# Kernel tuning notes

Measured on AMD Instinct MI355X. Metric: run time of the kernel, lower is better.

## Reference

```python
import jax, jax.numpy as jnp
import numpy as np

BETA = 0.25
EPS = 1e-12

def normalise(x):
    # L2 normalise over last axis
    return x / jnp.sqrt(jnp.sum(x * x, axis=-1, keepdims=True) + EPS)

def setup_inputs() -> dict:
    key = jax.random.key(0)
    k = jax.random.split(key, 6)
    N, d, c, P = 8192, 768, 256, 16384
    return {
        "z": jax.random.normal(k[0], (N, d), dtype=jnp.float32),
        "W_in": jax.random.normal(k[1], (d, c), dtype=jnp.float32) * 0.02,
        "b_in": jnp.zeros((c,), dtype=jnp.float32),
        "W_out": jax.random.normal(k[2], (c, d), dtype=jnp.float32) * 0.02,
        "b_out": jnp.zeros((d,), dtype=jnp.float32),
        "codebook": jax.random.normal(k[3], (P, c), dtype=jnp.float32),
    }

def reference(z, W_in, b_in, W_out, b_out, codebook):
    sg = jax.lax.stop_gradient
    # input projection + L2 normalise
    zq = normalise(z @ W_in + b_in)                 # [N, c]
    cb = normalise(codebook)                        # [P, c]
    # squared euclidean distances: ||z||^2 - 2 z.c + ||c||^2
    dist = (jnp.sum(zq * zq, axis=-1, keepdims=True)
            - 2.0 * jnp.einsum('nc,pc->np', zq, cb)
            + jnp.sum(cb * cb, axis=-1)[None, :])   # [N, P]
    idxes = jnp.argmin(dist, axis=-1)               # [N]
    codes = normalise(codebook[idxes])              # gather + normalise, [N, c]
    loss = BETA * (zq - sg(codes)) ** 2 + (sg(zq) - codes) ** 2
    # straight-through estimator
    codes = zq + sg(codes - zq)
    out = codes @ W_out + b_out                     # [N, d]
    return out, loss, idxes
```

## Files before the change

kernel.cpp:

```cpp
#include <hip/hip_runtime.h>
#include <hip/hip_fp16.h>
#include <math.h>

#define NN 8192
#define DD 768
#define CC 256
#define PP 16384
#define NG 256
#define MARGIN 5.0e-3f
#define BETA_C 1.25f
#define EPS_C 1e-12f

typedef __attribute__((ext_vector_type(8))) _Float16 f16x8;
typedef __attribute__((ext_vector_type(8))) short bf16x8;
typedef __attribute__((ext_vector_type(4))) float f32x4;
typedef __attribute__((ext_vector_type(16))) float f32x16;

static __device__ __forceinline__ ushort f2h(float x) {
    _Float16 h = (_Float16)x;
    return __builtin_bit_cast(unsigned short, h);
}
static __device__ __forceinline__ ushort f2bf(float x) {
    unsigned u = __float_as_uint(x);
    return (ushort)((u + 0x7fffu + ((u >> 16) & 1u)) >> 16);
}
static __device__ __forceinline__ float bf2f(ushort h) {
    return __uint_as_float(((unsigned)h) << 16);
}

static __device__ __forceinline__ void gload_lds16(const void* g, void* l) {
    __builtin_amdgcn_global_load_lds(
        (const __attribute__((address_space(1))) unsigned int*)g,
        (__attribute__((address_space(3))) unsigned int*)l, 16, 0, 0);
}

__global__ __launch_bounds__(256) void k_gemm_in(const float* __restrict__ z,
    const float* __restrict__ W, const float* __restrict__ b,
    float* __restrict__ zq)
{
    __shared__ float zt[64][36];
    __shared__ float wt[32][68];
    const int t = threadIdx.x;
    const int ti = t >> 4, tj = t & 15;
    const int n0 = blockIdx.x * 64;
    const int c0 = blockIdx.y * 64;

    f32x4 acc[4];
#pragma unroll
    for (int r = 0; r < 4; ++r) acc[r] = (f32x4){0.f, 0.f, 0.f, 0.f};

    for (int k0 = 0; k0 < DD; k0 += 32) {
        __syncthreads();
#pragma unroll
        for (int l = 0; l < 2; ++l) {
            int idx = l * 256 + t;
            int row = idx >> 3, c4 = idx & 7;
            *reinterpret_cast<float4*>(&zt[row][c4 * 4]) =
                *reinterpret_cast<const float4*>(&z[(size_t)(n0 + row) * DD + k0 + c4 * 4]);
            int krow = idx >> 4, w4 = idx & 15;
            *reinterpret_cast<float4*>(&wt[krow][w4 * 4]) =
                *reinterpret_cast<const float4*>(&W[(size_t)(k0 + krow) * CC + c0 + w4 * 4]);
        }
        __syncthreads();
#pragma unroll
        for (int kk = 0; kk < 32; kk += 4) {
            float4 a4[4], b4[4];
#pragma unroll
            for (int r = 0; r < 4; ++r)
                a4[r] = *reinterpret_cast<const float4*>(&zt[ti * 4 + r][kk]);
#pragma unroll
            for (int q = 0; q < 4; ++q)
                b4[q] = *reinterpret_cast<const float4*>(&wt[kk + q][tj * 4]);
#pragma unroll
            for (int q = 0; q < 4; ++q)
#pragma unroll
                for (int r = 0; r < 4; ++r) {
                    float av = ((const float*)&a4[r])[q];
                    acc[r].x += av * b4[q].x;
                    acc[r].y += av * b4[q].y;
                    acc[r].z += av * b4[q].z;
                    acc[r].w += av * b4[q].w;
                }
        }
    }
#pragma unroll
    for (int r = 0; r < 4; ++r) {
        int col = c0 + tj * 4;
        float4 o;
        o.x = acc[r].x + b[col];
        o.y = acc[r].y + b[col + 1];
        o.z = acc[r].z + b[col + 2];
        o.w = acc[r].w + b[col + 3];
        *reinterpret_cast<float4*>(&zq[(size_t)(n0 + ti * 4 + r) * CC + col]) = o;
    }
}

__global__ __launch_bounds__(256) void k_norm2(const float* __restrict__ src,
    float* __restrict__ dstf32, ushort* __restrict__ dsth,
    float* __restrict__ sq, float* __restrict__ rinvout, int rows)
{
    const int wave = threadIdx.x >> 6;
    const int lane = threadIdx.x & 63;
    const int row = blockIdx.x * 4 + wave;
    if (row >= rows) return;
    float4 v = *reinterpret_cast<const float4*>(&src[(size_t)row * CC + lane * 4]);
    float s = v.x * v.x + v.y * v.y + v.z * v.z + v.w * v.w;
#pragma unroll
    for (int off = 32; off; off >>= 1) s += __shfl_xor(s, off, 64);
    float r = 1.0f / sqrtf(s + EPS_C);
    v.x *= r; v.y *= r; v.z *= r; v.w *= r;
    if (dstf32)
        *reinterpret_cast<float4*>(&dstf32[(size_t)row * CC + lane * 4]) = v;
    ushort4 hv;
    hv.x = f2h(v.x); hv.y = f2h(v.y); hv.z = f2h(v.z); hv.w = f2h(v.w);
    *reinterpret_cast<ushort4*>(&dsth[(size_t)row * CC + lane * 4]) = hv;
    if (sq) {
        float s2 = v.x * v.x + v.y * v.y + v.z * v.z + v.w * v.w;
#pragma unroll
        for (int off = 32; off; off >>= 1) s2 += __shfl_xor(s2, off, 64);
        if (lane == 0) {
            sq[row] = s2;
            if (rinvout) rinvout[row] = r;
        }
    }
}

__global__ __launch_bounds__(256) void k_split_w(const float* __restrict__ W,
    ushort* __restrict__ wthi, ushort* __restrict__ wtlo)
{
    __shared__ float tile[64][68];
    const int t = threadIdx.x;
    const int d0 = blockIdx.x * 64;
    const int k0 = blockIdx.y * 64;
#pragma unroll
    for (int i = 0; i < 16; ++i) {
        int row = i * 4 + (t >> 6);
        int col = t & 63;
        tile[row][col] = W[(size_t)(k0 + row) * DD + d0 + col];
    }
    __syncthreads();
#pragma unroll
    for (int i = 0; i < 16; ++i) {
        int drow = i * 4 + (t >> 6);
        int kc = t & 63;
        float v = tile[kc][drow];
        ushort hi = f2bf(v);
        float rres = v - bf2f(hi);
        ushort lo = f2bf(rres);
        wthi[(size_t)(d0 + drow) * CC + k0 + kc] = hi;
        wtlo[(size_t)(d0 + drow) * CC + k0 + kc] = lo;
    }
}

__global__ __launch_bounds__(256) void k_dist(
    const ushort* __restrict__ cbh, const ushort* __restrict__ zqh,
    const float* __restrict__ cz2,
    float* __restrict__ gmin, unsigned long long* __restrict__ maskA)
{
    __shared__ ushort lA[256 * 64];
    __shared__ ushort lB[128 * 64];
    const int t = threadIdx.x;
    const int lane = t & 63;
    const int w = t >> 6;
    const int wr = w >> 1;
    const int wc = w & 1;
    const int p0 = blockIdx.x * 256;
    const int n0 = blockIdx.y * 128;
    const int kh = lane >> 5;
    const int r31 = lane & 31;

    f32x16 acc[4][2];
#pragma unroll
    for (int mi = 0; mi < 4; ++mi) {
        const int pbm = p0 + wr * 128 + mi * 32;
#pragma unroll
        for (int q = 0; q < 4; ++q) {
            float4 cz = *reinterpret_cast<const float4*>(&cz2[pbm + q * 8 + kh * 4]);
#pragma unroll
            for (int j = 0; j < 4; ++j) {
                float v = -0.5f * ((const float*)&cz.x)[j];
                acc[mi][0][q * 4 + j] = v;
                acc[mi][1][q * 4 + j] = v;
            }
        }
    }

    const int srow = lane >> 3;
    const int schunk = (lane & 7) ^ srow;
    const char* srcA = (const char*)cbh + (size_t)(p0 + w * 64 + srow) * (CC * 2) + schunk * 16;
    const char* srcB = (const char*)zqh + (size_t)(n0 + w * 32 + srow) * (CC * 2) + schunk * 16;
    char* dstA = (char*)lA + (w * 64) * 128;
    char* dstB = (char*)lB + (w * 32) * 128;

    const char* lAc = (const char*)lA;
    const char* lBc = (const char*)lB;
    const int sx = (r31 & 7) << 4;

    for (int k0 = 0; k0 < CC; k0 += 64) {
        __syncthreads();
#pragma unroll
        for (int i = 0; i < 8; ++i)
            gload_lds16(srcA + (size_t)i * 8 * (CC * 2) + k0 * 2, dstA + i * 1024);
#pragma unroll
        for (int i = 0; i < 4; ++i)
            gload_lds16(srcB + (size_t)i * 8 * (CC * 2) + k0 * 2, dstB + i * 1024);
        __syncthreads();
#pragma unroll
        for (int ks = 0; ks < 4; ++ks) {
            const int ko = ((ks * 32 + kh * 16) ^ sx);
            f16x8 af[4], bfv[2];
#pragma unroll
            for (int mi = 0; mi < 4; ++mi)
                af[mi] = *reinterpret_cast<const f16x8*>(
                    lAc + (wr * 128 + mi * 32 + r31) * 128 + ko);
#pragma unroll
            for (int ni = 0; ni < 2; ++ni)
                bfv[ni] = *reinterpret_cast<const f16x8*>(
                    lBc + (wc * 64 + ni * 32 + r31) * 128 + ko);
#pragma unroll
            for (int mi = 0; mi < 4; ++mi)
#pragma unroll
                for (int ni = 0; ni < 2; ++ni)
                    acc[mi][ni] = __builtin_amdgcn_mfma_f32_32x32x16_f16(
                        af[mi], bfv[ni], acc[mi][ni], 0, 0, 0);
        }
    }

#pragma unroll
    for (int ni = 0; ni < 2; ++ni) {
#pragma unroll
        for (int g = 0; g < 2; ++g) {
            float M = -1e30f;
#pragma unroll
            for (int m2 = 0; m2 < 2; ++m2)
#pragma unroll
                for (int r = 0; r < 16; ++r) M = fmaxf(M, acc[g * 2 + m2][ni][r]);
            M = fmaxf(M, __shfl_xor(M, 32, 64));
            const float thr = M - 0.5f * MARGIN;
            unsigned long long msk = 0ull;
#pragma unroll
            for (int m2 = 0; m2 < 2; ++m2)
#pragma unroll
                for (int q = 0; q < 4; ++q) {
                    unsigned nib = 0u;
#pragma unroll
                    for (int j = 0; j < 4; ++j)
                        nib |= (acc[g * 2 + m2][ni][q * 4 + j] >= thr) ? (1u << j) : 0u;
                    msk |= (unsigned long long)nib << (m2 * 32 + q * 8 + kh * 4);
                }
            msk |= __shfl_xor(msk, 32, 64);
            if (kh == 0) {
                int n = n0 + wc * 64 + ni * 32 + r31;
                int grp = (p0 >> 6) + wr * 2 + g;
                gmin[(size_t)n * NG + grp] = -2.0f * M;
                maskA[(size_t)n * NG + grp] = msk;
            }
        }
    }
}

__global__ __launch_bounds__(256) void k_pick(
    const float* __restrict__ gmin, const unsigned long long* __restrict__ maskA,
    const float* __restrict__ zqn, const float* __restrict__ cb_raw,
    const float* __restrict__ rinv, const float* __restrict__ cz2,
    float* __restrict__ idxf, int* __restrict__ idxi)
{
    __shared__ int lst[4][256];
    __shared__ int cnt[4];
    const int t = threadIdx.x;
    const int w = t >> 6;
    const int lane = t & 63;
    const int row = blockIdx.x * 4 + w;

    float4 zr = *reinterpret_cast<const float4*>(&zqn[(size_t)row * CC + lane * 4]);
    float4 gv = *reinterpret_cast<const float4*>(&gmin[(size_t)row * NG + lane * 4]);

    float pm = fminf(fminf(gv.x, gv.y), fminf(gv.z, gv.w));
#pragma unroll
    for (int off = 1; off < 64; off <<= 1) pm = fminf(pm, __shfl_xor(pm, off, 64));
    const float thresh = pm + MARGIN;

    if (lane == 0) cnt[w] = 0;
    __syncthreads();
    {
        const float g4[4] = {gv.x, gv.y, gv.z, gv.w};
#pragma unroll
        for (int j = 0; j < 4; ++j)
            if (g4[j] <= thresh) {
                int pos = atomicAdd(&cnt[w], 1);
                lst[w][pos] = lane * 4 + j;
            }
    }
    __syncthreads();

    const int nc = cnt[w];
    unsigned long long best = ~0ull;
    for (int ci = 0; ci < nc; ++ci) {
        int g = lst[w][ci];
        unsigned long long msk = maskA[(size_t)row * NG + g];
        while (msk) {
            int bit = __ffsll((long long)msk) - 1;
            msk &= msk - 1;
            int p = g * 64 + bit;
            float rv = rinv[p];
            float4 c4 = *reinterpret_cast<const float4*>(&cb_raw[(size_t)p * CC + lane * 4]);
            float part = (c4.x * rv) * zr.x + (c4.y * rv) * zr.y
                       + (c4.z * rv) * zr.z + (c4.w * rv) * zr.w;
#pragma unroll
            for (int off = 1; off < 64; off <<= 1) part += __shfl_xor(part, off, 64);
            float d4 = fmaf(-2.0f, part, 4.0f + cz2[p]);
            unsigned long long pk = ((unsigned long long)__float_as_uint(d4) << 32) | (unsigned)p;
            best = best < pk ? best : pk;
        }
    }
    if (lane == 0) {
        int p = (int)(best & 0xffffffffu);
        idxf[row] = (float)p;
        idxi[row] = p;
    }
}

__global__ __launch_bounds__(256) void k_codes(const float* __restrict__ zqn,
    const float* __restrict__ cb_raw, const float* __restrict__ rinv,
    const int* __restrict__ idxv, ushort* __restrict__ chi,
    ushort* __restrict__ clo, float* __restrict__ loss)
{
    int idx = blockIdx.x * 256 + threadIdx.x;
    int n = idx >> 6;
    int c4 = idx & 63;
    int p = idxv[n];
    float rv = rinv[p];
    float4 cv = *reinterpret_cast<const float4*>(&cb_raw[(size_t)p * CC + c4 * 4]);
    cv.x *= rv; cv.y *= rv; cv.z *= rv; cv.w *= rv;
    ushort4 hv, lv16;
    {
        hv.x = f2bf(cv.x); lv16.x = f2bf(cv.x - bf2f(hv.x));
        hv.y = f2bf(cv.y); lv16.y = f2bf(cv.y - bf2f(hv.y));
        hv.z = f2bf(cv.z); lv16.z = f2bf(cv.z - bf2f(hv.z));
        hv.w = f2bf(cv.w); lv16.w = f2bf(cv.w - bf2f(hv.w));
    }
    *reinterpret_cast<ushort4*>(&chi[(size_t)n * CC + c4 * 4]) = hv;
    *reinterpret_cast<ushort4*>(&clo[(size_t)n * CC + c4 * 4]) = lv16;
    float4 zv = *reinterpret_cast<const float4*>(&zqn[(size_t)n * CC + c4 * 4]);
    float4 lsv;
    float dx = zv.x - cv.x, dy = zv.y - cv.y, dz = zv.z - cv.z, dw = zv.w - cv.w;
    lsv.x = BETA_C * dx * dx; lsv.y = BETA_C * dy * dy;
    lsv.z = BETA_C * dz * dz; lsv.w = BETA_C * dw * dw;
    *reinterpret_cast<float4*>(&loss[(size_t)n * CC + c4 * 4]) = lsv;
}

__global__ __launch_bounds__(256) void k_gemm_out_mfma(
    const ushort* __restrict__ chi, const ushort* __restrict__ clo,
    const ushort* __restrict__ wthi, const ushort* __restrict__ wtlo,
    const float* __restrict__ bout, float* __restrict__ out)
{
    __shared__ ushort sAh[128 * 64];
    __shared__ ushort sAl[128 * 64];
    __shared__ ushort sBh[128 * 64];
    __shared__ ushort sBl[128 * 64];
    const int t = threadIdx.x;
    const int lane = t & 63;
    const int w = t >> 6;
    const int wr = w >> 1;
    const int wc = w & 1;
    const int nb = blockIdx.x * 128;
    const int db = blockIdx.y * 128;
    const int kh = lane >> 5;
    const int r31 = lane & 31;

    f32x16 acc[2][2];
#pragma unroll
    for (int mi = 0; mi < 2; ++mi)
#pragma unroll
        for (int ni = 0; ni < 2; ++ni)
#pragma unroll
            for (int r = 0; r < 16; ++r) acc[mi][ni][r] = 0.f;

    const int srow = lane >> 3;
    const int schunk = (lane & 7) ^ srow;
    const size_t rowA = (size_t)(nb + w * 32 + srow) * CC;
    const size_t rowB = (size_t)(db + w * 32 + srow) * CC;
    const char* sAhsrc = (const char*)chi + rowA * 2 + schunk * 16;
    const char* sAlsrc = (const char*)clo + rowA * 2 + schunk * 16;
    const char* sBhsrc = (const char*)wthi + rowB * 2 + schunk * 16;
    const char* sBlsrc = (const char*)wtlo + rowB * 2 + schunk * 16;
    char* dA = (char*)sAh + (w * 32) * 128;
    char* dAl = (char*)sAl + (w * 32) * 128;
    char* dB = (char*)sBh + (w * 32) * 128;
    char* dBl = (char*)sBl + (w * 32) * 128;

    const int sx = (r31 & 7) << 4;

    for (int k0 = 0; k0 < CC; k0 += 64) {
        __syncthreads();
#pragma unroll
        for (int i = 0; i < 4; ++i) {
            gload_lds16(sAhsrc + (size_t)i * 8 * (CC * 2) + k0 * 2, dA + i * 1024);
            gload_lds16(sAlsrc + (size_t)i * 8 * (CC * 2) + k0 * 2, dAl + i * 1024);
            gload_lds16(sBhsrc + (size_t)i * 8 * (CC * 2) + k0 * 2, dB + i * 1024);
            gload_lds16(sBlsrc + (size_t)i * 8 * (CC * 2) + k0 * 2, dBl + i * 1024);
        }
        __syncthreads();
#pragma unroll
        for (int ks = 0; ks < 4; ++ks) {
            const int ko = ((ks * 32 + kh * 16) ^ sx);
            bf16x8 ah[2], al[2], bh[2], bl[2];
#pragma unroll
            for (int mi = 0; mi < 2; ++mi) {
                ah[mi] = *reinterpret_cast<const bf16x8*>(
                    (const char*)sAh + (wr * 64 + mi * 32 + r31) * 128 + ko);
                al[mi] = *reinterpret_cast<const bf16x8*>(
                    (const char*)sAl + (wr * 64 + mi * 32 + r31) * 128 + ko);
            }
#pragma unroll
            for (int ni = 0; ni < 2; ++ni) {
                bh[ni] = *reinterpret_cast<const bf16x8*>(
                    (const char*)sBh + (wc * 64 + ni * 32 + r31) * 128 + ko);
                bl[ni] = *reinterpret_cast<const bf16x8*>(
                    (const char*)sBl + (wc * 64 + ni * 32 + r31) * 128 + ko);
            }
#pragma unroll
            for (int mi = 0; mi < 2; ++mi)
#pragma unroll
                for (int ni = 0; ni < 2; ++ni) {
                    acc[mi][ni] = __builtin_amdgcn_mfma_f32_32x32x16_bf16(
                        ah[mi], bh[ni], acc[mi][ni], 0, 0, 0);
                    acc[mi][ni] = __builtin_amdgcn_mfma_f32_32x32x16_bf16(
                        ah[mi], bl[ni], acc[mi][ni], 0, 0, 0);
                    acc[mi][ni] = __builtin_amdgcn_mfma_f32_32x32x16_bf16(
                        al[mi], bh[ni], acc[mi][ni], 0, 0, 0);
                }
        }
    }

#pragma unroll
    for (int ni = 0; ni < 2; ++ni) {
        const int d = db + wc * 64 + ni * 32 + r31;
        const float bv = bout[d];
#pragma unroll
        for (int mi = 0; mi < 2; ++mi) {
            const int nbase = nb + wr * 64 + mi * 32 + 4 * kh;
#pragma unroll
            for (int q = 0; q < 4; ++q)
#pragma unroll
                for (int j = 0; j < 4; ++j) {
                    int n = nbase + j + 8 * q;
                    out[(size_t)n * DD + d] = acc[mi][ni][q * 4 + j] + bv;
                }
        }
    }
}

extern "C" void kernel_launch(void* const* d_in, const int* in_sizes, int n_in,
                              void* d_out, int out_size, void* d_ws, size_t ws_size,
                              hipStream_t stream)
{
    const float* z        = (const float*)d_in[0];
    const float* W_in     = (const float*)d_in[1];
    const float* b_in     = (const float*)d_in[2];
    const float* W_out    = (const float*)d_in[3];
    const float* b_out    = (const float*)d_in[4];
    const float* codebook = (const float*)d_in[5];

    char* ws = (char*)d_ws;
    ushort* zqh   = (ushort*)(ws);
    ushort* cbh   = (ushort*)(ws + 4194304);
    ushort* chi   = (ushort*)(ws + 12582912);
    ushort* clo   = (ushort*)(ws + 16777216);
    ushort* wthi  = (ushort*)(ws + 20971520);
    ushort* wtlo  = (ushort*)(ws + 21364736);
    float*  cz2   = (float*)(ws + 21757952);
    float*  rinv  = (float*)(ws + 21823488);
    int*    idxi  = (int*)  (ws + 21889024);

    float* out  = (float*)d_out;
    float* loss = out + (size_t)NN * DD;
    float* idxf = loss + (size_t)NN * CC;

    float* gmin = (float*)d_out;
    unsigned long long* maskA = (unsigned long long*)((char*)d_out + 8388608);
    float* zq = loss;

    k_gemm_in<<<dim3(NN / 64, CC / 64), 256, 0, stream>>>(z, W_in, b_in, zq);
    k_norm2<<<NN / 4, 256, 0, stream>>>(zq, zq, zqh, (float*)nullptr, (float*)nullptr, NN);
    k_norm2<<<PP / 4, 256, 0, stream>>>(codebook, (float*)nullptr, cbh, cz2, rinv, PP);
    k_split_w<<<dim3(DD / 64, CC / 64), 256, 0, stream>>>(W_out, wthi, wtlo);
    k_dist<<<dim3(PP / 256, NN / 128), 256, 0, stream>>>(cbh, zqh, cz2, gmin, maskA);
    k_pick<<<NN / 4, 256, 0, stream>>>(gmin, maskA, zq, codebook, rinv, cz2, idxf, idxi);
    k_codes<<<(NN * CC / 4) / 256, 256, 0, stream>>>(zq, codebook, rinv, idxi, chi, clo, loss);
    k_gemm_out_mfma<<<dim3(NN / 128, DD / 128), 256, 0, stream>>>(chi, clo, wthi, wtlo, b_out, out);
}
```

Baseline: 183.2 us.

## Double-buffer LDS tiles in distance kernel with smaller K steps and MFMA priority

Changes the k_dist main loop from single-buffered 64-wide K tiles to double-buffered 32-wide K tiles. The next tile's global-to-LDS loads are issued while MFMAs run on the current buffer, and a new row-pair interleaved swizzled layout is used. MFMA issue is wrapped in s_setprio to favour the math wave. The intent is to hide global load latency and remove one barrier per iteration, at the cost of more loop iterations and the same LDS footprint (2x12288 halves).

```diff
diff --git a/kernel.cpp b/kernel.cpp
--- a/kernel.cpp
+++ b/kernel.cpp
@@ -157,8 +157,7 @@
     const float* __restrict__ cz2,
     float* __restrict__ gmin, unsigned long long* __restrict__ maskA)
 {
-    __shared__ ushort lA[256 * 64];
-    __shared__ ushort lB[128 * 64];
+    __shared__ ushort lds[2][12288];
     const int t = threadIdx.x;
     const int lane = t & 63;
     const int w = t >> 6;
@@ -185,46 +184,65 @@
         }
     }
 
-    const int srow = lane >> 3;
-    const int schunk = (lane & 7) ^ srow;
-    const char* srcA = (const char*)cbh + (size_t)(p0 + w * 64 + srow) * (CC * 2) + schunk * 16;
-    const char* srcB = (const char*)zqh + (size_t)(n0 + w * 32 + srow) * (CC * 2) + schunk * 16;
-    char* dstA = (char*)lA + (w * 64) * 128;
-    char* dstB = (char*)lB + (w * 32) * 128;
-
-    const char* lAc = (const char*)lA;
-    const char* lBc = (const char*)lB;
-    const int sx = (r31 & 7) << 4;
-
-    for (int k0 = 0; k0 < CC; k0 += 64) {
-        __syncthreads();
-#pragma unroll
-        for (int i = 0; i < 8; ++i)
-            gload_lds16(srcA + (size_t)i * 8 * (CC * 2) + k0 * 2, dstA + i * 1024);
-#pragma unroll
-        for (int i = 0; i < 4; ++i)
-            gload_lds16(srcB + (size_t)i * 8 * (CC * 2) + k0 * 2, dstB + i * 1024);
-        __syncthreads();
-#pragma unroll
-        for (int ks = 0; ks < 4; ++ks) {
-            const int ko = ((ks * 32 + kh * 16) ^ sx);
+    const int u_l = lane >> 3;
+    const int e = (lane & 7) ^ u_l;
+    const int hh = e >> 2, jj = e & 3;
+    const ushort* srcA[4];
+    const ushort* srcB[2];
+#pragma unroll
+    for (int i = 0; i < 4; ++i)
+        srcA[i] = cbh + (size_t)(p0 + 2 * (w * 32 + i * 8 + u_l) + hh) * CC + jj * 8;
+#pragma unroll
+    for (int i = 0; i < 2; ++i)
+        srcB[i] = zqh + (size_t)(n0 + 2 * (w * 16 + i * 8 + u_l) + hh) * CC + jj * 8;
+
+#define STAGE(buf, kt)                                                        \
+    {                                                                         \
+        _Pragma("unroll")                                                     \
+        for (int i = 0; i < 4; ++i)                                           \
+            gload_lds16(srcA[i] + (kt) * 32, &lds[buf][(w * 32 + i * 8) * 64]); \
+        _Pragma("unroll")                                                     \
+        for (int i = 0; i < 2; ++i)                                           \
+            gload_lds16(srcB[i] + (kt) * 32, &lds[buf][8192 + (w * 16 + i * 8) * 64]); \
+    }
+
+    const int ua = wr * 64 + (r31 >> 1);
+    const int ub = wc * 32 + (r31 >> 1);
+    const int hb = (r31 & 1) * 4 + kh;
+
+    STAGE(0, 0);
+    __syncthreads();
+
+    for (int kt = 0; kt < 8; ++kt) {
+        const int cur = kt & 1;
+        if (kt < 7) STAGE(cur ^ 1, kt + 1);
+#pragma unroll
+        for (int ks = 0; ks < 2; ++ks) {
             f16x8 af[4], bfv[2];
 #pragma unroll
-            for (int mi = 0; mi < 4; ++mi)
+            for (int mi = 0; mi < 4; ++mi) {
+                int u = ua + mi * 16;
                 af[mi] = *reinterpret_cast<const f16x8*>(
-                    lAc + (wr * 128 + mi * 32 + r31) * 128 + ko);
-#pragma unroll
-            for (int ni = 0; ni < 2; ++ni)
+                    &lds[cur][u * 64 + (((hb + ks * 2) ^ (u & 7)) * 8)]);
+            }
+#pragma unroll
+            for (int ni = 0; ni < 2; ++ni) {
+                int u = ub + ni * 16;
                 bfv[ni] = *reinterpret_cast<const f16x8*>(
-                    lBc + (wc * 64 + ni * 32 + r31) * 128 + ko);
+                    &lds[cur][8192 + u * 64 + (((hb + ks * 2) ^ (u & 7)) * 8)]);
+            }
+            __builtin_amdgcn_s_setprio(1);
 #pragma unroll
             for (int mi = 0; mi < 4; ++mi)
 #pragma unroll
                 for (int ni = 0; ni < 2; ++ni)
                     acc[mi][ni] = __builtin_amdgcn_mfma_f32_32x32x16_f16(
                         af[mi], bfv[ni], acc[mi][ni], 0, 0, 0);
-        }
-    }
+            __builtin_amdgcn_s_setprio(0);
+        }
+        if (kt < 7) __syncthreads();
+    }
+#undef STAGE
 
 #pragma unroll
     for (int ni = 0; ni < 2; ++ni) {
```

Result: slower. 189.0 us (+3.1%).
